# Performance work log

Measured on AMD Instinct MI355X. Metric: run time of the kernel, lower is better.

Reference implementation:

```python
import jax, jax.numpy as jnp
import numpy as np

MAX_DISP = 4  # PWC-Net correlation: displacements in [-4,4] -> 9x9 = 81 channels


def setup_inputs() -> dict:
    key = jax.random.key(0)
    k1, k2 = jax.random.split(key)
    B, C, H, W = 8, 128, 112, 192
    tensorFirst = jax.random.normal(k1, (B, C, H, W), dtype=jnp.float32)
    tensorSecond = jax.random.normal(k2, (B, C, H, W), dtype=jnp.float32)
    return {"tensorFirst": tensorFirst, "tensorSecond": tensorSecond}


def reference(tensorFirst, tensorSecond):
    B, C, H, W = tensorFirst.shape
    D = MAX_DISP
    # zero-pad second by max displacement on each spatial side (rbot padding of 8 = 2*4)
    padded = jnp.pad(tensorSecond, ((0, 0), (0, 0), (D, D), (D, D)))
    outs = []
    # fixed 9x9 displacement grid; channel index = (dy+4)*9 + (dx+4)
    for dy in range(2 * D + 1):
        for dx in range(2 * D + 1):
            shifted = jax.lax.dynamic_slice(padded, (0, 0, dy, dx), (B, C, H, W))
            # dot product over channels, normalized by C (sumelems in the cupy kernel)
            outs.append(jnp.mean(tensorFirst * shifted, axis=1))
    return jnp.stack(outs, axis=1)  # [B, 81, H, W]
```

## Files before the change

kernel.cpp:

```cpp
#include <hip/hip_runtime.h>


typedef __attribute__((ext_vector_type(8))) short bf16x8;
typedef __attribute__((ext_vector_type(4))) float f32x4;

namespace {
constexpr int kC = 128, kH = 112, kW = 192;
constexpr int kHW = kH * kW;
constexpr long long kCHW = (long long)kC * kHW;
constexpr int YT = 8;
constexpr int XT = 16;
constexpr int NS = 32;
constexpr int YS = 16;
constexpr int KC = 32;
constexpr int NT = 384;
constexpr int A_YSTRIDE = XT * KC * 2;
constexpr int B_YSTRIDE = NS * KC * 2;
constexpr int B_OFF = YT * A_YSTRIDE;
constexpr int LDS_BYTES = B_OFF + YS * B_YSTRIDE;
constexpr int A_SLOTS = YT * XT * (KC / 8);
constexpr int B_SLOTS = YS * NS * (KC / 8);
}

__device__ __forceinline__ unsigned pack2_bf16(float a, float b) {
  unsigned ua = __float_as_uint(a) + 0x8000u;
  unsigned ub = __float_as_uint(b) + 0x8000u;
  return (ua >> 16) | (ub & 0xffff0000u);
}

__global__ __launch_bounds__(NT, 3)
void corr81_mfma(const float* __restrict__ first,
                 const float* __restrict__ second,
                 float* __restrict__ out) {
  __shared__ uint4 lds4[LDS_BYTES / 16];
  unsigned char* lds = (unsigned char*)lds4;

  const int g = blockIdx.x;
  const int b = g & 7;
  const int i = g >> 3;
  const int xt = i % (kW / XT);
  const int yt = i / (kW / XT);
  const int x0 = xt * XT, y0 = yt * YT;

  const int tid = threadIdx.x;
  const int lane = tid & 63;
  const int wv = tid >> 6;
  const int dy_w = (wv % 3) * 3;
  const int y_w = (wv / 3) * 4;
  const int col = lane & 15;
  const int q = lane >> 4;

  f32x4 acc[4][3][2];
#pragma unroll
  for (int yy = 0; yy < 4; ++yy)
#pragma unroll
    for (int dd = 0; dd < 3; ++dd)
#pragma unroll
      for (int nh = 0; nh < 2; ++nh) acc[yy][dd][nh] = (f32x4){0.f, 0.f, 0.f, 0.f};

  const float* fb = first + (long long)b * kCHW;
  const float* sb = second + (long long)b * kCHW;

  for (int ck = 0; ck < kC / KC; ++ck) {
    const int c0 = ck * KC;
    __syncthreads();

    for (int s = tid; s < A_SLOTS + B_SLOTS; s += NT) {
      if (s < A_SLOTS) {
        const int kg = s & 3, xl = (s >> 2) & 15, yl = s >> 6;
        const float* p = fb + (long long)(c0 + kg * 8) * kHW +
                         (y0 + yl) * kW + (x0 + xl);
        uint4 w;
        w.x = pack2_bf16(p[0], p[kHW]);
        w.y = pack2_bf16(p[2 * kHW], p[3 * kHW]);
        w.z = pack2_bf16(p[4 * kHW], p[5 * kHW]);
        w.w = pack2_bf16(p[6 * kHW], p[7 * kHW]);
        *(uint4*)(lds + yl * A_YSTRIDE + xl * (KC * 2) + kg * 16) = w;
      } else {
        const int t = s - A_SLOTS;
        const int kg = t & 3, n = (t >> 2) & 31, ys = t >> 7;
        const int ysg = y0 + ys - 4;
        const int xsg = x0 + n - 4;
        uint4 w = make_uint4(0u, 0u, 0u, 0u);
        if ((unsigned)ysg < (unsigned)kH && (unsigned)xsg < (unsigned)kW) {
          const float* p = sb + (long long)(c0 + kg * 8) * kHW +
                           ysg * kW + xsg;
          w.x = pack2_bf16(p[0], p[kHW]);
          w.y = pack2_bf16(p[2 * kHW], p[3 * kHW]);
          w.z = pack2_bf16(p[4 * kHW], p[5 * kHW]);
          w.w = pack2_bf16(p[6 * kHW], p[7 * kHW]);
        }
        *(uint4*)(lds + B_OFF + ys * B_YSTRIDE + n * (KC * 2) + kg * 16) = w;
      }
    }
    __syncthreads();

    bf16x8 aF[4];
#pragma unroll
    for (int yy = 0; yy < 4; ++yy)
      aF[yy] = *(const bf16x8*)(lds + (y_w + yy) * A_YSTRIDE + col * (KC * 2) +
                                q * 16);
    const int sbase = y_w + dy_w;
#pragma unroll
    for (int nh = 0; nh < 2; ++nh) {
      bf16x8 bF[6];
#pragma unroll
      for (int si = 0; si < 6; ++si)
        bF[si] = *(const bf16x8*)(lds + B_OFF + (sbase + si) * B_YSTRIDE +
                                  (nh * 16 + col) * (KC * 2) + q * 16);
#pragma unroll
      for (int yy = 0; yy < 4; ++yy)
#pragma unroll
        for (int dd = 0; dd < 3; ++dd)
          acc[yy][dd][nh] = __builtin_amdgcn_mfma_f32_16x16x32_bf16(
              aF[yy], bF[yy + dd], acc[yy][dd][nh], 0, 0, 0);
    }
  }

  const float scale = 1.f / 128.f;
#pragma unroll
  for (int nh = 0; nh < 2; ++nh)
#pragma unroll
    for (int r = 0; r < 4; ++r) {
      const int xloc = q * 4 + r;
      const int d = nh * 16 + col - xloc;
      if ((unsigned)d <= 8u) {
#pragma unroll
        for (int yy = 0; yy < 4; ++yy)
#pragma unroll
          for (int dd = 0; dd < 3; ++dd) {
            const int ch = (dy_w + dd) * 9 + d;
            const long long o =
                (((long long)b * 81 + ch) * kH + (y0 + y_w + yy)) *
                    (long long)kW +
                (x0 + xloc);
            out[o] = acc[yy][dd][nh][r] * scale;
          }
      }
    }
}

extern "C" void kernel_launch(void* const* d_in, const int* in_sizes, int n_in,
                              void* d_out, int out_size, void* d_ws, size_t ws_size,
                              hipStream_t stream) {
  const float* first = (const float*)d_in[0];
  const float* second = (const float*)d_in[1];
  float* out = (float*)d_out;

  const int grid = 8 * (kH / YT) * (kW / XT);
  corr81_mfma<<<grid, NT, 0, stream>>>(first, second, out);
}
```

Baseline: 334.0 us.

## Use float4 global loads with channel-pair LDS layout and y-major block order

Global loads switch from scalar per-channel gathers to float4 loads along x, with pairs of channels packed into bf16x2 dwords. Shared memory moves to a channel-pair-major layout, so each MFMA fragment is assembled from four scalar LDS dword reads instead of one 16-byte read. Block indexing now walks y tiles first, which may improve L2 reuse of overlapping halo rows, and launch bounds drop to 2 blocks per CU. The aim is to cut the number of global memory transactions, at the price of more LDS read instructions and lower occupancy.

After: 365.5 us. 9.4% more time.

```diff
diff --git a/kernel.cpp b/kernel.cpp
--- a/kernel.cpp
+++ b/kernel.cpp
@@ -10,16 +10,10 @@
 constexpr long long kCHW = (long long)kC * kHW;
 constexpr int YT = 8;
 constexpr int XT = 16;
-constexpr int NS = 32;
-constexpr int YS = 16;
 constexpr int KC = 32;
 constexpr int NT = 384;
-constexpr int A_YSTRIDE = XT * KC * 2;
-constexpr int B_YSTRIDE = NS * KC * 2;
-constexpr int B_OFF = YT * A_YSTRIDE;
-constexpr int LDS_BYTES = B_OFF + YS * B_YSTRIDE;
-constexpr int A_SLOTS = YT * XT * (KC / 8);
-constexpr int B_SLOTS = YS * NS * (KC / 8);
+constexpr int A_DW = 8 * 16 * 16;
+constexpr int B_DW = 16 * 16 * 32;
 }
 
 __device__ __forceinline__ unsigned pack2_bf16(float a, float b) {
@@ -28,18 +22,17 @@
   return (ua >> 16) | (ub & 0xffff0000u);
 }
 
-__global__ __launch_bounds__(NT, 3)
+__global__ __launch_bounds__(NT, 2)
 void corr81_mfma(const float* __restrict__ first,
                  const float* __restrict__ second,
                  float* __restrict__ out) {
-  __shared__ uint4 lds4[LDS_BYTES / 16];
-  unsigned char* lds = (unsigned char*)lds4;
+  __shared__ unsigned lds32[A_DW + B_DW];
 
   const int g = blockIdx.x;
   const int b = g & 7;
   const int i = g >> 3;
-  const int xt = i % (kW / XT);
-  const int yt = i / (kW / XT);
+  const int yt = i % (kH / YT);
+  const int xt = i / (kH / YT);
   const int x0 = xt * XT, y0 = yt * YT;
 
   const int tid = threadIdx.x;
@@ -65,49 +58,72 @@
     const int c0 = ck * KC;
     __syncthreads();
 
-    for (int s = tid; s < A_SLOTS + B_SLOTS; s += NT) {
-      if (s < A_SLOTS) {
-        const int kg = s & 3, xl = (s >> 2) & 15, yl = s >> 6;
-        const float* p = fb + (long long)(c0 + kg * 8) * kHW +
-                         (y0 + yl) * kW + (x0 + xl);
+#pragma unroll
+    for (int k = 0; k < 2; ++k) {
+      const int s = tid + k * NT;
+      if (s < 512) {
+        const int xq = s & 3, y = (s >> 2) & 7, cp = s >> 5;
+        const float* p = fb + (long long)(c0 + 2 * cp) * kHW +
+                         (y0 + y) * kW + x0 + xq * 4;
+        const float4 a = *(const float4*)p;
+        const float4 c = *(const float4*)(p + kHW);
         uint4 w;
-        w.x = pack2_bf16(p[0], p[kHW]);
-        w.y = pack2_bf16(p[2 * kHW], p[3 * kHW]);
-        w.z = pack2_bf16(p[4 * kHW], p[5 * kHW]);
-        w.w = pack2_bf16(p[6 * kHW], p[7 * kHW]);
-        *(uint4*)(lds + yl * A_YSTRIDE + xl * (KC * 2) + kg * 16) = w;
-      } else {
-        const int t = s - A_SLOTS;
-        const int kg = t & 3, n = (t >> 2) & 31, ys = t >> 7;
+        w.x = pack2_bf16(a.x, c.x);
+        w.y = pack2_bf16(a.y, c.y);
+        w.z = pack2_bf16(a.z, c.z);
+        w.w = pack2_bf16(a.w, c.w);
+        *(uint4*)&lds32[(y * 16 + cp) * 16 + xq * 4] = w;
+      }
+    }
+
+#pragma unroll
+    for (int k = 0; k < 6; ++k) {
+      const int s = tid + k * NT;
+      if (s < 2048) {
+        const int xq = s & 7, ys = (s >> 3) & 15, cp = s >> 7;
         const int ysg = y0 + ys - 4;
-        const int xsg = x0 + n - 4;
+        const int xsg = x0 - 4 + xq * 4;
         uint4 w = make_uint4(0u, 0u, 0u, 0u);
         if ((unsigned)ysg < (unsigned)kH && (unsigned)xsg < (unsigned)kW) {
-          const float* p = sb + (long long)(c0 + kg * 8) * kHW +
+          const float* p = sb + (long long)(c0 + 2 * cp) * kHW +
                            ysg * kW + xsg;
-          w.x = pack2_bf16(p[0], p[kHW]);
-          w.y = pack2_bf16(p[2 * kHW], p[3 * kHW]);
-          w.z = pack2_bf16(p[4 * kHW], p[5 * kHW]);
-          w.w = pack2_bf16(p[6 * kHW], p[7 * kHW]);
+          const float4 a = *(const float4*)p;
+          const float4 c = *(const float4*)(p + kHW);
+          w.x = pack2_bf16(a.x, c.x);
+          w.y = pack2_bf16(a.y, c.y);
+          w.z = pack2_bf16(a.z, c.z);
+          w.w = pack2_bf16(a.w, c.w);
         }
-        *(uint4*)(lds + B_OFF + ys * B_YSTRIDE + n * (KC * 2) + kg * 16) = w;
+        *(uint4*)&lds32[A_DW + (ys * 16 + cp) * 32 + xq * 4] = w;
       }
     }
     __syncthreads();
 
     bf16x8 aF[4];
 #pragma unroll
-    for (int yy = 0; yy < 4; ++yy)
-      aF[yy] = *(const bf16x8*)(lds + (y_w + yy) * A_YSTRIDE + col * (KC * 2) +
-                                q * 16);
+    for (int yy = 0; yy < 4; ++yy) {
+      const int base = ((y_w + yy) * 16 + q * 4) * 16 + col;
+      uint4 v;
+      v.x = lds32[base];
+      v.y = lds32[base + 16];
+      v.z = lds32[base + 32];
+      v.w = lds32[base + 48];
+      aF[yy] = __builtin_bit_cast(bf16x8, v);
+    }
     const int sbase = y_w + dy_w;
 #pragma unroll
     for (int nh = 0; nh < 2; ++nh) {
       bf16x8 bF[6];
 #pragma unroll
-      for (int si = 0; si < 6; ++si)
-        bF[si] = *(const bf16x8*)(lds + B_OFF + (sbase + si) * B_YSTRIDE +
-                                  (nh * 16 + col) * (KC * 2) + q * 16);
+      for (int si = 0; si < 6; ++si) {
+        const int base = A_DW + ((sbase + si) * 16 + q * 4) * 32 + nh * 16 + col;
+        uint4 v;
+        v.x = lds32[base];
+        v.y = lds32[base + 32];
+        v.z = lds32[base + 64];
+        v.w = lds32[base + 96];
+        bF[si] = __builtin_bit_cast(bf16x8, v);
+      }
 #pragma unroll
       for (int yy = 0; yy < 4; ++yy)
 #pragma unroll
```
